# Kernel tuning notes

Hardware: AMD Instinct MI355X
Metric: run time of the kernel (lower is better)

The kernel has to match this reference:

```python
import jax, jax.numpy as jnp
import numpy as np

EPS = 1e-6

def setup_inputs() -> dict:
    key = jax.random.key(0)
    k1, k2, k3, k4, k5, k6 = jax.random.split(key, 6)
    B, S, N_IMG, D = 4, 4096, 2048, 2048
    encoder = jax.random.normal(k1, (B, S, D), dtype=jnp.float32)
    objectness = jax.random.normal(k2, (B, N_IMG), dtype=jnp.float32)
    boxes = jax.random.uniform(k3, (B, N_IMG, 4), dtype=jnp.float32)
    # learned parameters
    gamma = jnp.ones((D,), dtype=jnp.float32) + 0.02 * jax.random.normal(k4, (D,), dtype=jnp.float32)  # T5LayerNorm weight
    w = jax.random.normal(k5, (D,), dtype=jnp.float32) / np.sqrt(D)  # Linear(n_in, 1) weight, flattened
    b = jax.random.normal(k6, (), dtype=jnp.float32) * 0.01          # Linear bias
    return {"encoder": encoder, "objectness": objectness, "boxes": boxes,
            "gamma": gamma, "w": w, "b": b}

def reference(encoder, objectness, boxes, gamma, w, b):
    # n_images = boxes.shape[1]; slice candidate regions
    n_images = boxes.shape[1]
    x = encoder[:, :n_images]                                  # [B, n_images, D]
    # T5LayerNorm: RMS normalization (no mean subtraction), scale by gamma
    variance = jnp.mean(jnp.square(x), axis=-1, keepdims=True)  # [B, n_images, 1]
    x_norm = x * jax.lax.rsqrt(variance + EPS) * gamma          # [B, n_images, D]
    # Linear(D, 1) -> squeeze(-1): a GEMV over the feature axis
    image_rel = jnp.einsum('bnd,d->bn', x_norm, w) + b          # [B, n_images]
    return image_rel
```

## Files before the change

### kernel.cpp

```cpp
#include <hip/hip_runtime.h>

#define EPS 1e-6f

template<int D>
__global__ __launch_bounds__(256, 4) void lo_kernel(
    const float* __restrict__ enc,
    const float* __restrict__ gamma,
    const float* __restrict__ w,
    const float* __restrict__ bias,
    float* __restrict__ out,
    int N_IMG, int S, int n_rows)
{
    const int lane = threadIdx.x & 63;
    const int row  = blockIdx.x * 4 + (threadIdx.x >> 6);
    if (row >= n_rows) return;

    const int b = row / N_IMG;
    const int n = row % N_IMG;
    const float* __restrict__ x = enc + ((size_t)b * S + n) * (size_t)D;

    constexpr int ITER = D / 256;

    float sumsq = 0.f, dot = 0.f;
    #pragma unroll
    for (int i = 0; i < ITER; ++i) {
        const int idx = i * 256 + lane * 4;
        const float4 xv = *reinterpret_cast<const float4*>(x + idx);
        const float4 gv = *reinterpret_cast<const float4*>(gamma + idx);
        const float4 wv = *reinterpret_cast<const float4*>(w + idx);
        sumsq = fmaf(xv.x, xv.x, fmaf(xv.y, xv.y, fmaf(xv.z, xv.z, fmaf(xv.w, xv.w, sumsq))));
        dot  = fmaf(xv.x * gv.x, wv.x,
               fmaf(xv.y * gv.y, wv.y,
               fmaf(xv.z * gv.z, wv.z,
               fmaf(xv.w * gv.w, wv.w, dot))));
    }

    #pragma unroll
    for (int o = 32; o > 0; o >>= 1) {
        sumsq += __shfl_xor(sumsq, o, 64);
        dot   += __shfl_xor(dot,   o, 64);
    }

    if (lane == 0) {
        const float inv = rsqrtf(sumsq * (1.0f / (float)D) + EPS);
        out[row] = dot * inv + bias[0];
    }
}

__global__ __launch_bounds__(256) void lo_kernel_generic(
    const float* __restrict__ enc,
    const float* __restrict__ gamma,
    const float* __restrict__ w,
    const float* __restrict__ bias,
    float* __restrict__ out,
    int N_IMG, int S, int D)
{
    const int row = blockIdx.x;
    const int b   = row / N_IMG;
    const int n   = row % N_IMG;
    const float* __restrict__ x = enc + ((size_t)b * S + n) * (size_t)D;
    const int t = threadIdx.x;

    float sumsq = 0.f, dot = 0.f;
    for (int d = t; d < D; d += 256) {
        const float xv = x[d];
        sumsq = fmaf(xv, xv, sumsq);
        dot   = fmaf(xv * gamma[d], w[d], dot);
    }
    #pragma unroll
    for (int o = 32; o > 0; o >>= 1) {
        sumsq += __shfl_xor(sumsq, o, 64);
        dot   += __shfl_xor(dot,   o, 64);
    }
    __shared__ float s_sq[4], s_dot[4];
    const int wid = t >> 6, lane = t & 63;
    if (lane == 0) { s_sq[wid] = sumsq; s_dot[wid] = dot; }
    __syncthreads();
    if (t == 0) {
        float ss = s_sq[0] + s_sq[1] + s_sq[2] + s_sq[3];
        float dd = s_dot[0] + s_dot[1] + s_dot[2] + s_dot[3];
        out[row] = dd * rsqrtf(ss / (float)D + EPS) + bias[0];
    }
}

extern "C" void kernel_launch(void* const* d_in, const int* in_sizes, int n_in,
                              void* d_out, int out_size, void* d_ws, size_t ws_size,
                              hipStream_t stream) {
    const float* enc   = (const float*)d_in[0];
    const float* gamma = (const float*)d_in[3];
    const float* w     = (const float*)d_in[4];
    const float* bias  = (const float*)d_in[5];
    float* out         = (float*)d_out;

    const int D      = in_sizes[3];
    const int B      = 4;
    const int BN     = in_sizes[1];
    const int N_IMG  = BN / B;
    const int S      = in_sizes[0] / (B * D);
    const int n_rows = out_size;

    if (D == 2048) {
        const int blocks = (n_rows + 3) / 4;
        lo_kernel<2048><<<blocks, 256, 0, stream>>>(enc, gamma, w, bias, out,
                                                    N_IMG, S, n_rows);
    } else {
        lo_kernel_generic<<<n_rows, 256, 0, stream>>>(enc, gamma, w, bias, out,
                                                      N_IMG, S, D);
    }
}
```

Baseline: 15.80 us.

## Process two rows per wave with precomputed gamma*w and nontemporal loads

Each wave now handles two rows and loads gamma and w once, folding them into a gamma*w register array that both rows reuse. This halves the parameter traffic per row and removes one multiply per element. Encoder loads use nontemporal hints, and partial sums are kept in vector accumulators. In exchange there are half as many waves and more registers per thread, which may lower occupancy and latency hiding on a bandwidth-bound 64MB read.

```diff
diff --git a/kernel.cpp b/kernel.cpp
--- a/kernel.cpp
+++ b/kernel.cpp
@@ -2,7 +2,9 @@
 
 #define EPS 1e-6f
 
-template<int D>
+using f4 = __attribute__((ext_vector_type(4))) float;
+
+template<int D, int R>
 __global__ __launch_bounds__(256, 4) void lo_kernel(
     const float* __restrict__ enc,
     const float* __restrict__ gamma,
@@ -11,39 +13,54 @@
     float* __restrict__ out,
     int N_IMG, int S, int n_rows)
 {
+    constexpr int ITER = D / 256;
     const int lane = threadIdx.x & 63;
-    const int row  = blockIdx.x * 4 + (threadIdx.x >> 6);
-    if (row >= n_rows) return;
+    const int wid  = threadIdx.x >> 6;
+    const int wave = blockIdx.x * 4 + wid;
+    const int row0 = wave * R;
+    if (row0 >= n_rows) return;
 
-    const int b = row / N_IMG;
-    const int n = row % N_IMG;
-    const float* __restrict__ x = enc + ((size_t)b * S + n) * (size_t)D;
+    const int col = lane * 4;
 
-    constexpr int ITER = D / 256;
-
-    float sumsq = 0.f, dot = 0.f;
+    f4 gw[ITER];
     #pragma unroll
     for (int i = 0; i < ITER; ++i) {
-        const int idx = i * 256 + lane * 4;
-        const float4 xv = *reinterpret_cast<const float4*>(x + idx);
-        const float4 gv = *reinterpret_cast<const float4*>(gamma + idx);
-        const float4 wv = *reinterpret_cast<const float4*>(w + idx);
-        sumsq = fmaf(xv.x, xv.x, fmaf(xv.y, xv.y, fmaf(xv.z, xv.z, fmaf(xv.w, xv.w, sumsq))));
-        dot  = fmaf(xv.x * gv.x, wv.x,
-               fmaf(xv.y * gv.y, wv.y,
-               fmaf(xv.z * gv.z, wv.z,
-               fmaf(xv.w * gv.w, wv.w, dot))));
+        const int idx = i * 256 + col;
+        const f4 gv = *reinterpret_cast<const f4*>(gamma + idx);
+        const f4 wv = *reinterpret_cast<const f4*>(w + idx);
+        gw[i] = gv * wv;
     }
 
+    const float bb = bias[0];
+
     #pragma unroll
-    for (int o = 32; o > 0; o >>= 1) {
-        sumsq += __shfl_xor(sumsq, o, 64);
-        dot   += __shfl_xor(dot,   o, 64);
-    }
+    for (int r = 0; r < R; ++r) {
+        const int row = row0 + r;
+        if (row >= n_rows) break;
+        const int b = row / N_IMG;
+        const int n = row - b * N_IMG;
+        const float* __restrict__ x = enc + ((size_t)b * S + n) * (size_t)D;
 
-    if (lane == 0) {
-        const float inv = rsqrtf(sumsq * (1.0f / (float)D) + EPS);
-        out[row] = dot * inv + bias[0];
+        f4 sq = {0.f, 0.f, 0.f, 0.f};
+        f4 dt = {0.f, 0.f, 0.f, 0.f};
+        #pragma unroll
+        for (int i = 0; i < ITER; ++i) {
+            const f4 xv = __builtin_nontemporal_load(
+                reinterpret_cast<const f4*>(x + i * 256 + col));
+            sq += xv * xv;
+            dt += xv * gw[i];
+        }
+
+        float ssq = sq.x + sq.y + sq.z + sq.w;
+        float ddt = dt.x + dt.y + dt.z + dt.w;
+        #pragma unroll
+        for (int o = 32; o > 0; o >>= 1) {
+            ssq += __shfl_xor(ssq, o, 64);
+            ddt += __shfl_xor(ddt, o, 64);
+        }
+        if (lane == 0) {
+            out[row] = ddt * rsqrtf(ssq * (1.0f / (float)D) + EPS) + bb;
+        }
     }
 }
 
@@ -100,9 +117,11 @@
     const int n_rows = out_size;
 
     if (D == 2048) {
-        const int blocks = (n_rows + 3) / 4;
-        lo_kernel<2048><<<blocks, 256, 0, stream>>>(enc, gamma, w, bias, out,
-                                                    N_IMG, S, n_rows);
+        constexpr int R = 2;
+        const int waves  = (n_rows + R - 1) / R;
+        const int blocks = (waves + 3) / 4;
+        lo_kernel<2048, R><<<blocks, 256, 0, stream>>>(enc, gamma, w, bias, out,
+                                                       N_IMG, S, n_rows);
     } else {
         lo_kernel_generic<<<n_rows, 256, 0, stream>>>(enc, gamma, w, bias, out,
                                                       N_IMG, S, D);
```

Result: no change. 15.71 us (median of 2 runs) (-0.6%).
